# Kernel optimization log

Measured on AMD Instinct MI355X. Metric: run time of the kernel, lower is better.

## Reference

```python
import jax, jax.numpy as jnp
import numpy as np

B, T, D = 4, 1024, 768
HW = 32            # H = W = sqrt(T)
DS = D // 16       # d_state = 48
CHUNK = 8          # items_each_chunk (must divide W)


def _ln(x, w, b, eps=1e-5):
    mu = x.mean(-1, keepdims=True)
    var = ((x - mu) ** 2).mean(-1, keepdims=True)
    return (x - mu) / jnp.sqrt(var + eps) * w + b


def _conv1x1(x, w):  # x: (B,C,H,W), w: (O,C)
    return jnp.einsum('bchw,oc->bohw', x, w)


def _dwconv(x, w, b, pad):  # depthwise conv, w: (C,1,k,k)
    y = jax.lax.conv_general_dilated(
        x, w, (1, 1), [(pad, pad), (pad, pad)],
        dimension_numbers=('NCHW', 'OIHW', 'NCHW'),
        feature_group_count=x.shape[1])
    if b is not None:
        y = y + b[None, :, None, None]
    return y


def _norm_gates(Gl, Gm, Gr):
    gl, gm, gr = jax.nn.sigmoid(Gl), jax.nn.sigmoid(Gm), jax.nn.sigmoid(Gr)
    s = gl + gm + gr
    s = s.at[:, :, 0, :].set(gm[:, :, 0, :] + gr[:, :, 0, :])    # top row: no h-1 neighbor
    s = s.at[:, :, -1, :].set(gl[:, :, -1, :] + gm[:, :, -1, :])  # bottom row: no h+1 neighbor
    s = jnp.maximum(s, 1e-7)
    return gl / s, gm / s, gr / s


def _gspn_scan(X, L, Gl, Gm, Gr, chunk):
    # GateRecurrent2dnoind: scan along W in independent chunks of `chunk` columns.
    # H[:, :, h, t] = L*X + Gl*Hprev[h-1] + Gm*Hprev[h] + Gr*Hprev[h+1], Hprev=0 at chunk start.
    b, c, h, w = X.shape
    nc = w // chunk

    def to_scan(a):  # (B,C,H,W) -> (chunk, B, C, H, nc)
        return a.reshape(b, c, h, nc, chunk).transpose(4, 0, 1, 2, 3)

    xs, ls, gls, gms, grs = map(to_scan, (X, L, Gl, Gm, Gr))

    def step(hprev, inp):
        x, l, gl, gm, gr = inp
        h_up = jnp.pad(hprev[:, :, :-1], ((0, 0), (0, 0), (1, 0), (0, 0)))
        h_dn = jnp.pad(hprev[:, :, 1:], ((0, 0), (0, 0), (0, 1), (0, 0)))
        hn = l * x + gl * h_up + gm * hprev + gr * h_dn
        return hn, hn

    _, ys = jax.lax.scan(step, jnp.zeros((b, c, h, nc), X.dtype), (xs, ls, gls, gms, grs))
    return ys.transpose(1, 2, 3, 4, 0).reshape(b, c, h, w)


def setup_inputs() -> dict:
    key = jax.random.key(0)
    ks = jax.random.split(key, 16)
    s = 0.02
    return {
        'hidden_states': jax.random.normal(ks[0], (B, T, D), jnp.float32),
        'norm_w': jnp.ones((D,), jnp.float32),
        'norm_b': jnp.zeros((D,), jnp.float32),
        'in_proj_w': jax.random.normal(ks[1], (D, D), jnp.float32) * s,
        'conv7_w': jax.random.normal(ks[2], (D, 1, 7, 7), jnp.float32) * s,
        'conv7_b': jnp.zeros((D,), jnp.float32),
        'xdown_w': jax.random.normal(ks[3], (DS, D), jnp.float32) * s,
        'wup_w': jax.random.normal(ks[4], (12 * D, DS), jnp.float32) * s,
        'lup_w': jax.random.normal(ks[5], (4 * D, DS), jnp.float32) * s,
        'uup_w': jax.random.normal(ks[6], (4 * D, DS), jnp.float32) * s,
        'dcoef_w': jax.random.normal(ks[7], (4 * D, DS), jnp.float32) * s,
        'm_w': jax.random.normal(ks[8], (4,), jnp.float32) * 0.25,
        'outconv_w': jax.random.normal(ks[9], (D, D), jnp.float32) * s,
        'outdconv_w': jax.random.normal(ks[10], (D, 1, 3, 3), jnp.float32) * s,
        'outproj_w': jax.random.normal(ks[11], (D, D), jnp.float32) * s,
    }


def reference(hidden_states, norm_w, norm_b, in_proj_w, conv7_w, conv7_b,
              xdown_w, wup_w, lup_w, uup_w, dcoef_w, m_w,
              outconv_w, outdconv_w, outproj_w):
    b, t, d = hidden_states.shape
    hh = ww = HW
    shortcut = hidden_states
    x = _ln(shortcut, norm_w, norm_b)                      # (B,T,D)
    x = x.transpose(0, 2, 1).reshape(b, d, hh, ww)         # (B,D,H,W)
    x = _conv1x1(x, in_proj_w)
    x = _dwconv(x, conv7_w, conv7_b, 3)
    xp = _conv1x1(x, xdown_w)                              # (B,ds,H,W)
    ws = _conv1x1(xp, wup_w)                               # (B,12D,H,W)
    Ls = _conv1x1(xp, lup_w)                               # (B,4D,H,W)
    Us = _conv1x1(xp, uup_w)
    Ds = _conv1x1(xp, dcoef_w)
    # 4 scan directions: [x, x^T, flip_w(x), flip_w(x^T)]
    x_hwwh = jnp.stack([x, x.transpose(0, 1, 3, 2)], axis=1)       # (B,2,D,H,W)
    xs = jnp.concatenate([x_hwwh, x_hwwh[..., ::-1]], axis=1)      # (B,4,D,H,W)
    xs = xs.reshape(b, 4 * d, hh, ww)
    Gl, Gm, Gr = ws[:, :4 * d], ws[:, 4 * d:8 * d], ws[:, 8 * d:]
    gl, gm, gr = _norm_gates(Gl, Gm, Gr)
    out = _gspn_scan(xs, Ls, gl, gm, gr, CHUNK)
    out = out * Us + xs * Ds
    out = out.reshape(b, 4, d, hh, ww)
    out = jnp.einsum('bkdhw,k->bdhw', out, m_w)            # m_conv (1x1 over 4 dirs)
    out = _conv1x1(out, outconv_w)
    out = _dwconv(out, outdconv_w, None, 1)
    out = out * jax.nn.relu(out)
    out = out.reshape(b, d, t).transpose(0, 2, 1)
    out = out @ outproj_w.T
    return out, shortcut
```

## Files before the change

kernel.cpp:

```cpp
#include <hip/hip_runtime.h>

typedef unsigned short u16;
typedef unsigned int u32;
typedef __attribute__((ext_vector_type(8))) short short8v;
typedef __attribute__((ext_vector_type(4))) float f32x4;
typedef __attribute__((ext_vector_type(2))) unsigned u32x2v;

#define DD 768
#define PP 1024
#define NTOK 4096

__device__ __forceinline__ u16 f2bf(float f) {
  u32 u = __builtin_bit_cast(u32, f);
  u += 0x7fffu + ((u >> 16) & 1u);
  return (u16)(u >> 16);
}
__device__ __forceinline__ float b2f(u16 v) {
  return __builtin_bit_cast(float, (u32)v << 16);
}
__device__ __forceinline__ u32 pk_trunc(float fa, float fb) {
  return __builtin_amdgcn_perm(__builtin_bit_cast(u32, fa), __builtin_bit_cast(u32, fb), 0x07060302u);
}
__device__ __forceinline__ float ex8(const short8v& v, int j) {
  const u32 dw = ((const u32*)&v)[j >> 1];
  return __builtin_bit_cast(float, (j & 1) ? (dw & 0xffff0000u) : (dw << 16));
}
__device__ __forceinline__ float dpp_shr1(float x) {
  return __builtin_bit_cast(float,
      __builtin_amdgcn_update_dpp(0, __builtin_bit_cast(int, x), 0x138, 0xf, 0xf, true));
}
__device__ __forceinline__ float dpp_shl1(float x) {
  return __builtin_bit_cast(float,
      __builtin_amdgcn_update_dpp(0, __builtin_bit_cast(int, x), 0x130, 0xf, 0xf, true));
}
__device__ __forceinline__ float xhalf_sum(float p) {
#if __has_builtin(__builtin_amdgcn_permlane32_swap)
  u32x2v sw = __builtin_amdgcn_permlane32_swap(__builtin_bit_cast(u32, p),
                                               __builtin_bit_cast(u32, p), false, false);
  return __builtin_bit_cast(float, sw[0]) + __builtin_bit_cast(float, sw[1]);
#else
  return p + __shfl_xor(p, 32, 64);
#endif
}

__global__ __launch_bounds__(256) void prep_ln_k(const float* __restrict__ hs,
                                                 const float* __restrict__ gw, const float* __restrict__ gb,
                                                 u16* __restrict__ lnout, float* __restrict__ shortcut,
                                                 const float* __restrict__ win, u16* __restrict__ wInB,
                                                 const float* __restrict__ wout, u16* __restrict__ wOutB,
                                                 const float* __restrict__ wprj, u16* __restrict__ wPrjB,
                                                 const float* __restrict__ xdw, u16* __restrict__ wXdB,
                                                 const float* __restrict__ wup, const float* __restrict__ lup,
                                                 const float* __restrict__ uup, const float* __restrict__ dco,
                                                 u16* __restrict__ wB) {
  const int id = blockIdx.x;
  const int t = threadIdx.x;
  if (id < 4096) {
    const int tok = id;
    const float* xr = hs + (size_t)tok * DD;
    float v0 = xr[t], v1 = xr[t + 256], v2 = xr[t + 512];
    float s = v0 + v1 + v2;
    float q = v0 * v0 + v1 * v1 + v2 * v2;
#pragma unroll
    for (int off = 32; off > 0; off >>= 1) {
      s += __shfl_down(s, off, 64);
      q += __shfl_down(q, off, 64);
    }
    __shared__ float ss[4], qs[4];
    const int wid = t >> 6, lane = t & 63;
    if (lane == 0) { ss[wid] = s; qs[wid] = q; }
    __syncthreads();
    const float st = ss[0] + ss[1] + ss[2] + ss[3];
    const float qt = qs[0] + qs[1] + qs[2] + qs[3];
    const float mu = st * (1.f / 768.f);
    const float var = qt * (1.f / 768.f) - mu * mu;
    const float rstd = rsqrtf(var + 1e-5f);
    float* sc = shortcut + (size_t)tok * DD;
    u16* lo = lnout + (size_t)tok * DD;
    sc[t] = v0; sc[t + 256] = v1; sc[t + 512] = v2;
    lo[t]       = f2bf((v0 - mu) * rstd * gw[t] + gb[t]);
    lo[t + 256] = f2bf((v1 - mu) * rstd * gw[t + 256] + gb[t + 256]);
    lo[t + 512] = f2bf((v2 - mu) * rstd * gw[t + 512] + gb[t + 512]);
    return;
  }
  const int id2 = id - 4096;
  if (id2 < 1728) {
    const int m = id2 / 576;
    const int i = (id2 - m * 576) * 1024 + t * 4;
    const float* s = (m == 0) ? win : (m == 1) ? wout : wprj;
    u16* d = (m == 0) ? wInB : (m == 1) ? wOutB : wPrjB;
    const float4 v = *reinterpret_cast<const float4*>(s + i);
    u16 o[4] = {f2bf(v.x), f2bf(v.y), f2bf(v.z), f2bf(v.w)};
    *reinterpret_cast<uint2*>(d + i) = *reinterpret_cast<const uint2*>(o);
  } else if (id2 < 1776) {
    const int i = (id2 - 1728) * 1024 + t * 4;
    const int r = i / DD;
    if (r < 48) {
      const float4 v = *reinterpret_cast<const float4*>(xdw + i);
      u16 o[4] = {f2bf(v.x), f2bf(v.y), f2bf(v.z), f2bf(v.w)};
      *reinterpret_cast<uint2*>(wXdB + i) = *reinterpret_cast<const uint2*>(o);
    } else {
      *reinterpret_cast<uint2*>(wXdB + i) = make_uint2(0u, 0u);
    }
  } else {
    const int c = id2 - 1776;
    u16* dst = wB + (size_t)c * 2048;
    for (int i = t; i < 2048; i += 256) {
      const int row = i >> 6, s = i & 63;
      u16 v = 0;
      if (row < 24 && s < 48) {
        const int k = row & 3, type = row >> 2;
        const int ch = k * DD + c;
        const float* src;
        if (type < 3) src = wup + ((size_t)(type * 3072 + ch)) * 48;
        else if (type == 3) src = lup + (size_t)ch * 48;
        else if (type == 4) src = uup + (size_t)ch * 48;
        else src = dco + (size_t)ch * 48;
        v = f2bf(src[s]);
      }
      dst[i] = v;
    }
  }
}

template <int BSRC>
__global__ __launch_bounds__(256) void gemm_bf16(const u16* __restrict__ A,
                                                 const u16* __restrict__ Bt,
                                                 void* __restrict__ outv, const int mode) {
  __shared__ u16 Al[64][72];
  __shared__ u16 BlF[71 * 72];
  const int t = threadIdx.x;
  const int ntile = blockIdx.x * 64;
  const int mtile = blockIdx.y * 64;
  const int bb = ntile >> 10, pq0 = ntile & 1023;
  const int wid = t >> 6, lane = t & 63;
  const int m0 = (wid & 1) * 32, n0 = (wid >> 1) * 32;
  const int l15 = lane & 15, quad = lane >> 4;
  f32x4 acc[2][2];
#pragma unroll
  for (int mi = 0; mi < 2; ++mi)
#pragma unroll
    for (int ni = 0; ni < 2; ++ni) acc[mi][ni] = (f32x4){0.f, 0.f, 0.f, 0.f};
  const int ra = t >> 2, sa = t & 3;
  const u16* ag = A + (size_t)(mtile + ra) * DD + sa * 16;
  const int rb = t >> 2, hb = t & 3;
  const u16* bg = Bt + (size_t)(ntile + rb) * DD + hb * 16;
  const int chp = t >> 3, tok0 = (t & 7) * 8;
  const u16* bgc0 = Bt + ((size_t)(bb * DD + chp * 2)) * PP + pq0 + tok0;
  const u16* bgc1 = bgc0 + PP;
  uint4 pa0, pa1, pb0, pb1;
#define LOADK(k0)                                                              \
  {                                                                            \
    pa0 = *reinterpret_cast<const uint4*>(ag + (k0));                          \
    pa1 = *reinterpret_cast<const uint4*>(ag + (k0) + 8);                      \
    if (BSRC == 0) {                                                           \
      pb0 = *reinterpret_cast<const uint4*>(bg + (k0));                        \
      pb1 = *reinterpret_cast<const uint4*>(bg + (k0) + 8);                    \
    } else {                                                                   \
      pb0 = *reinterpret_cast<const uint4*>(bgc0 + (size_t)(k0) * PP);         \
      pb1 = *reinterpret_cast<const uint4*>(bgc1 + (size_t)(k0) * PP);         \
    }                                                                          \
  }
  LOADK(0);
  for (int k0 = 0; k0 < DD; k0 += 64) {
    __syncthreads();
    *reinterpret_cast<uint4*>(&Al[ra][sa * 16]) = pa0;
    *reinterpret_cast<uint4*>(&Al[ra][sa * 16 + 8]) = pa1;
    if (BSRC == 0) {
      const int pr = rb + (rb >> 3);
      *reinterpret_cast<uint4*>(&BlF[pr * 72 + hb * 16]) = pb0;
      *reinterpret_cast<uint4*>(&BlF[pr * 72 + hb * 16 + 8]) = pb1;
    } else {
      union { uint4 v; u16 u[8]; } ua, ub;
      ua.v = pb0; ub.v = pb1;
#pragma unroll
      for (int i2 = 0; i2 < 8; ++i2) {
        const int tk = tok0 + i2;
        const int prow = (tk + (tk >> 3)) * 72;
        *reinterpret_cast<u32*>(&BlF[prow + chp * 2]) =
            (u32)ua.u[i2] | ((u32)ub.u[i2] << 16);
      }
    }
    __syncthreads();
    if (k0 + 64 < DD) LOADK(k0 + 64);
    short8v af[2][2], bfr[2][2];
#pragma unroll
    for (int mi = 0; mi < 2; ++mi)
#pragma unroll
      for (int ks = 0; ks < 2; ++ks)
        af[mi][ks] = *reinterpret_cast<const short8v*>(&Al[m0 + mi * 16 + l15][ks * 32 + quad * 8]);
#pragma unroll
    for (int ni = 0; ni < 2; ++ni) {
      const int tl = n0 + ni * 16 + l15;
      const int prow = (tl + (tl >> 3)) * 72;
#pragma unroll
      for (int ks = 0; ks < 2; ++ks)
        bfr[ni][ks] = *reinterpret_cast<const short8v*>(&BlF[prow + ks * 32 + quad * 8]);
    }
#pragma unroll
    for (int mi = 0; mi < 2; ++mi)
#pragma unroll
      for (int ni = 0; ni < 2; ++ni) {
        acc[mi][ni] = __builtin_amdgcn_mfma_f32_16x16x32_bf16(af[mi][0], bfr[ni][0], acc[mi][ni], 0, 0, 0);
        acc[mi][ni] = __builtin_amdgcn_mfma_f32_16x16x32_bf16(af[mi][1], bfr[ni][1], acc[mi][ni], 0, 0, 0);
      }
  }
#undef LOADK
  if (mode == 1) {
#pragma unroll
    for (int mi = 0; mi < 2; ++mi)
#pragma unroll
      for (int ni = 0; ni < 2; ++ni) {
        const int ob = mtile + m0 + mi * 16 + quad * 4;
        const int pg = ntile + n0 + ni * 16 + l15;
        *reinterpret_cast<f32x4*>((float*)outv + (size_t)pg * DD + ob) = acc[mi][ni];
      }
  } else {
    __syncthreads();
#pragma unroll
    for (int mi = 0; mi < 2; ++mi)
#pragma unroll
      for (int ni = 0; ni < 2; ++ni)
#pragma unroll
        for (int r = 0; r < 4; ++r)
          BlF[(m0 + mi * 16 + quad * 4 + r) * 72 + n0 + ni * 16 + l15] = f2bf(acc[mi][ni][r]);
    __syncthreads();
    const int orow = t >> 2, oc0 = (t & 3) * 16;
    const uint4 o0 = *reinterpret_cast<const uint4*>(&BlF[orow * 72 + oc0]);
    const uint4 o1 = *reinterpret_cast<const uint4*>(&BlF[orow * 72 + oc0 + 8]);
    u16* dstb = (u16*)outv + ((size_t)(bb * DD + mtile + orow)) * PP + pq0 + oc0;
    *reinterpret_cast<uint4*>(dstb) = o0;
    *reinterpret_cast<uint4*>(dstb + 8) = o1;
  }
}

__global__ __launch_bounds__(256) void xdgemm_k(const u16* __restrict__ A,
                                                const u16* __restrict__ Ycm,
                                                u16* __restrict__ xpA) {
  __shared__ u16 Al[64][72];
  __shared__ u16 Bl[16][72];
  const int t = threadIdx.x;
  const int ntile = blockIdx.x * 16;
  const int bb = ntile >> 10, pq0 = ntile & 1023;
  const int wid = t >> 6, lane = t & 63, l15 = lane & 15, quad = lane >> 4;
  f32x4 acc = (f32x4){0.f, 0.f, 0.f, 0.f};
  const int arow = t >> 2, aks = (t & 3) * 16;
  const u16* ag = A + (size_t)arow * DD + aks;
  const int chp = t >> 3;
  const int tk0 = (t & 7) * 2;
  const u16* bg0 = Ycm + ((size_t)(bb * DD + chp * 2)) * PP + pq0 + tk0;
  uint4 pa0, pa1;
  u32 pb0, pb1;
#define LOADX(k0)                                                     \
  {                                                                   \
    pa0 = *reinterpret_cast<const uint4*>(ag + (k0));                 \
    pa1 = *reinterpret_cast<const uint4*>(ag + (k0) + 8);             \
    pb0 = *reinterpret_cast<const u32*>(bg0 + (size_t)(k0) * PP);     \
    pb1 = *reinterpret_cast<const u32*>(bg0 + (size_t)((k0) + 1) * PP); \
  }
  LOADX(0);
  for (int k0 = 0; k0 < DD; k0 += 64) {
    __syncthreads();
    *reinterpret_cast<uint4*>(&Al[arow][aks]) = pa0;
    *reinterpret_cast<uint4*>(&Al[arow][aks + 8]) = pa1;
    *reinterpret_cast<u32*>(&Bl[tk0][chp * 2]) = (pb0 & 0xffffu) | (pb1 << 16);
    *reinterpret_cast<u32*>(&Bl[tk0 + 1][chp * 2]) = (pb0 >> 16) | (pb1 & 0xffff0000u);
    __syncthreads();
    if (k0 + 64 < DD) LOADX(k0 + 64);
#pragma unroll
    for (int ks = 0; ks < 2; ++ks) {
      const short8v af = *reinterpret_cast<const short8v*>(&Al[wid * 16 + l15][ks * 32 + quad * 8]);
      const short8v bf = *reinterpret_cast<const short8v*>(&Bl[l15][ks * 32 + quad * 8]);
      acc = __builtin_amdgcn_mfma_f32_16x16x32_bf16(af, bf, acc, 0, 0, 0);
    }
  }
#undef LOADX
  const int pq = pq0 + l15;
  const int i = ((pq & 31) >> 4) * 512 + (pq >> 5) * 16 + (pq & 15);
  u16* dst = xpA + ((size_t)(bb * 1024 + i)) * 64 + wid * 16 + quad * 4;
  *reinterpret_cast<uint2*>(dst) = make_uint2(pk_trunc(acc[1], acc[0]), pk_trunc(acc[3], acc[2]));
}

__global__ __launch_bounds__(256) void dwconv7_k(const u16* __restrict__ x,
                                                 const float* __restrict__ wgt,
                                                 const float* __restrict__ bias,
                                                 u16* __restrict__ y) {
  const int bc = blockIdx.x;
  const int c = bc % DD;
  __shared__ float tile[38 * 38];
  __shared__ float wl[49];
  __shared__ float bsh[1];
  const int t = threadIdx.x;
  for (int i = t; i < 38 * 38; i += 256) tile[i] = 0.f;
  __syncthreads();
  const u16* xr = x + (size_t)bc * PP;
  for (int i = t; i < 512; i += 256) {
    const u32 v = reinterpret_cast<const u32*>(xr)[i];
    const int p0 = i * 2;
    const int h = p0 >> 5, w = p0 & 31;
    tile[(h + 3) * 38 + w + 3] = b2f((u16)v);
    tile[(h + 3) * 38 + w + 4] = b2f((u16)(v >> 16));
  }
  if (t < 49) wl[t] = wgt[c * 49 + t];
  if (t == 0) bsh[0] = bias[c];
  __syncthreads();
  u16* yo = y + (size_t)bc * PP;
  const int w = t & 31, hb = t >> 5;
  const float bv = bsh[0];
  float a0 = bv, a1 = bv, a2 = bv, a3 = bv;
#pragma unroll
  for (int rr = 0; rr < 10; ++rr) {
    float row[7];
#pragma unroll
    for (int kw = 0; kw < 7; ++kw) row[kw] = tile[(hb * 4 + rr) * 38 + w + kw];
    if (rr < 7) {
#pragma unroll
      for (int kw = 0; kw < 7; ++kw) a0 = fmaf(wl[rr * 7 + kw], row[kw], a0);
    }
    if (rr >= 1 && rr < 8) {
#pragma unroll
      for (int kw = 0; kw < 7; ++kw) a1 = fmaf(wl[(rr - 1) * 7 + kw], row[kw], a1);
    }
    if (rr >= 2 && rr < 9) {
#pragma unroll
      for (int kw = 0; kw < 7; ++kw) a2 = fmaf(wl[(rr - 2) * 7 + kw], row[kw], a2);
    }
    if (rr >= 3) {
#pragma unroll
      for (int kw = 0; kw < 7; ++kw) a3 = fmaf(wl[(rr - 3) * 7 + kw], row[kw], a3);
    }
  }
  yo[(hb * 4 + 0) * 32 + w] = f2bf(a0);
  yo[(hb * 4 + 1) * 32 + w] = f2bf(a1);
  yo[(hb * 4 + 2) * 32 + w] = f2bf(a2);
  yo[(hb * 4 + 3) * 32 + w] = f2bf(a3);
}

__global__ __launch_bounds__(256) void dwconv3_k(const u16* __restrict__ x,
                                                 const float* __restrict__ wgt,
                                                 u16* __restrict__ y) {
  const int bc = blockIdx.x;
  const int c = bc % DD;
  __shared__ float tile[34 * 34];
  __shared__ float wl[9];
  const int t = threadIdx.x;
  for (int i = t; i < 34 * 34; i += 256) tile[i] = 0.f;
  __syncthreads();
  const u16* xr = x + (size_t)bc * PP;
  for (int i = t; i < 512; i += 256) {
    const u32 v = reinterpret_cast<const u32*>(xr)[i];
    const int p0 = i * 2;
    const int h = p0 >> 5, w = p0 & 31;
    tile[(h + 1) * 34 + w + 1] = b2f((u16)v);
    tile[(h + 1) * 34 + w + 2] = b2f((u16)(v >> 16));
  }
  if (t < 9) wl[t] = wgt[c * 9 + t];
  __syncthreads();
  u16* yo = y + (size_t)bc * PP;
  const int w = t & 31, hb = t >> 5;
  float a0 = 0.f, a1 = 0.f, a2 = 0.f, a3 = 0.f;
#pragma unroll
  for (int rr = 0; rr < 6; ++rr) {
    float row[3];
#pragma unroll
    for (int kw = 0; kw < 3; ++kw) row[kw] = tile[(hb * 4 + rr) * 34 + w + kw];
    if (rr < 3) {
#pragma unroll
      for (int kw = 0; kw < 3; ++kw) a0 = fmaf(wl[rr * 3 + kw], row[kw], a0);
    }
    if (rr >= 1 && rr < 4) {
#pragma unroll
      for (int kw = 0; kw < 3; ++kw) a1 = fmaf(wl[(rr - 1) * 3 + kw], row[kw], a1);
    }
    if (rr >= 2 && rr < 5) {
#pragma unroll
      for (int kw = 0; kw < 3; ++kw) a2 = fmaf(wl[(rr - 2) * 3 + kw], row[kw], a2);
    }
    if (rr >= 3) {
#pragma unroll
      for (int kw = 0; kw < 3; ++kw) a3 = fmaf(wl[(rr - 3) * 3 + kw], row[kw], a3);
    }
  }
  const float r0 = a0 > 0.f ? a0 * a0 : 0.f;
  const float r1 = a1 > 0.f ? a1 * a1 : 0.f;
  const float r2 = a2 > 0.f ? a2 * a2 : 0.f;
  const float r3 = a3 > 0.f ? a3 * a3 : 0.f;
  yo[(hb * 4 + 0) * 32 + w] = f2bf(r0);
  yo[(hb * 4 + 1) * 32 + w] = f2bf(r1);
  yo[(hb * 4 + 2) * 32 + w] = f2bf(r2);
  yo[(hb * 4 + 3) * 32 + w] = f2bf(r3);
}

#define ACT_SWZ(row, col) ((col) ^ (((((col) >> 6) ^ (row)) & 7) << 3))
#define PSWZ(r) ((((r) ^ ((r) >> 3)) & 3) << 3)

__device__ __forceinline__ void produce_half(u16* __restrict__ actbuf,
                                             const u16* __restrict__ ab,
                                             const short8v bw[2][2],
                                             int l15, int quad, int g) {
#pragma unroll
  for (int mt = 0; mt < 8; ++mt) {
    const u16* ar = ab + (mt * 16 + l15) * 64 + quad * 8;
    const short8v a0 = *reinterpret_cast<const short8v*>(ar);
    const short8v a1 = *reinterpret_cast<const short8v*>(ar + 32);
    f32x4 acc0 = {0.f, 0.f, 0.f, 0.f}, acc1 = {0.f, 0.f, 0.f, 0.f};
    acc0 = __builtin_amdgcn_mfma_f32_16x16x32_bf16(a0, bw[0][0], acc0, 0, 0, 0);
    acc0 = __builtin_amdgcn_mfma_f32_16x16x32_bf16(a1, bw[0][1], acc0, 0, 0, 0);
    acc1 = __builtin_amdgcn_mfma_f32_16x16x32_bf16(a0, bw[1][0], acc1, 0, 0, 0);
    acc1 = __builtin_amdgcn_mfma_f32_16x16x32_bf16(a1, bw[1][1], acc1, 0, 0, 0);
    const int qb = g * 128 + mt * 16 + quad * 4;
    const int cs = ACT_SWZ(l15, qb);
    *reinterpret_cast<uint2*>(&actbuf[l15 * 512 + cs]) =
        make_uint2(pk_trunc(acc0[1], acc0[0]), pk_trunc(acc0[3], acc0[2]));
    if (l15 < 8)
      *reinterpret_cast<uint2*>(&actbuf[(16 + l15) * 512 + cs]) =
          make_uint2(pk_trunc(acc1[1], acc1[0]), pk_trunc(acc1[3], acc1[2]));
  }
}

__device__ __forceinline__ void consume_half(const u16* __restrict__ actbuf,
                                             const u16* __restrict__ planeTc,
                                             const u16* __restrict__ y2row,
                                             u16* __restrict__ outpc,
                                             float mw, int dpair, int cs2, int d, int h, int half) {
  __builtin_amdgcn_s_setprio(1);
  const int k = dpair * 2 + d;
  const int hc = half * 2 + cs2;
  const int colb = h * 16 + cs2 * 8;
  const int wst = dpair ? (24 - hc * 8) : (hc * 8);
  short8v vPr;
  if (d == 0) vPr = *reinterpret_cast<const short8v*>(y2row + h * 32 + wst);
  else        vPr = *reinterpret_cast<const short8v*>(planeTc + h * 40 + (wst ^ PSWZ(h)));
  short8v vPe;
  {
    const u32* s = (const u32*)&vPr;
    u32* dq = (u32*)&vPe;
    if (dpair) {
      dq[0] = (s[3] >> 16) | (s[3] << 16);
      dq[1] = (s[2] >> 16) | (s[2] << 16);
      dq[2] = (s[1] >> 16) | (s[1] << 16);
      dq[3] = (s[0] >> 16) | (s[0] << 16);
    } else {
      dq[0] = s[0]; dq[1] = s[1]; dq[2] = s[2]; dq[3] = s[3];
    }
  }
#define ACTP(row) (*reinterpret_cast<const short8v*>(&actbuf[(row) * 512 + ACT_SWZ((row), colb)]))
  const short8v vGl = ACTP(0 + k);
  const short8v vGm = ACTP(4 + k);
  const short8v vGr = ACTP(8 + k);
  const short8v vL  = ACTP(12 + k);
  const short8v vU  = ACTP(16 + k);
  const short8v vD  = ACTP(20 + k);
#undef ACTP
  const bool top = (h == 0), bot = (h == 31);
  float H = 0.f, prev = 0.f;
  u32 ox[4];
#pragma unroll
  for (int j = 0; j < 8; ++j) {
    float el = __expf(-ex8(vGl, j));
    const float em = __expf(-ex8(vGm, j));
    float er = __expf(-ex8(vGr, j));
    if (top) el = 1e30f;
    if (bot) er = 1e30f;
    const float pl2 = 1.f + el, pm = 1.f + em, pr = 1.f + er;
    const float ul = pm * pr, um = pl2 * pr, ur = pl2 * pm;
    const float rcpS = __builtin_amdgcn_rcpf(ul + um + ur);
    const float xv = ex8(vPe, j);
    const float Lx = ex8(vL, j) * xv;
    const float up = dpp_shr1(H);
    const float dn = dpp_shl1(H);
    H = fmaf(ul * rcpS, up, fmaf(um * rcpS, H, fmaf(ur * rcpS, dn, Lx)));
    float part = fmaf(H, ex8(vU, j), xv * ex8(vD, j)) * mw;
    part = xhalf_sum(part);
    if (j & 1) ox[j >> 1] = pk_trunc(part, prev);
    else prev = part;
  }
  if (d == 0) {
    uint4 o;
    o.x = ox[0]; o.y = ox[1]; o.z = ox[2]; o.w = ox[3];
    *reinterpret_cast<uint4*>(&outpc[h * 64 + dpair * 32 + ((hc * 8) ^ ((h & 3) << 3))]) = o;
  }
  __builtin_amdgcn_s_setprio(0);
}

__global__ __launch_bounds__(512, 4) void scan_k(const u16* __restrict__ y2b,
                                                 const u16* __restrict__ xpA,
                                                 const u16* __restrict__ wB,
                                                 const float* __restrict__ mwp,
                                                 u16* __restrict__ out1) {
  const int bc2 = blockIdx.x;
  const int b = bc2 / 384;
  const int cpair = bc2 - b * 384;
  const int c0 = cpair * 2;
  __shared__ __align__(16) u16 actA[24 * 512];
  __shared__ __align__(16) u16 actB[24 * 512];
  __shared__ __align__(16) u16 planeT[2][1280];
  __shared__ __align__(16) u16 outp[2][32 * 64];
  const int t = threadIdx.x;
  const int wid = t >> 6, lane = t & 63, l15 = lane & 15, quad = lane >> 4;
  const int ch = wid >> 2;
  const int g = wid & 3;
  const int dpair = g & 1, cs2 = g >> 1;
  const int d = lane >> 5, h = lane & 31;
  const int c = c0 + ch;
  const int bc = b * DD + c;
  {
    const int pch = t >> 8, idx = t & 255;
    const u16* yp = y2b + (size_t)(b * DD + c0 + pch) * PP;
#pragma unroll
    for (int i2 = 0; i2 < 2; ++i2) {
      const int i = idx + i2 * 256;
      const u32 v = reinterpret_cast<const u32*>(yp)[i];
      const int p0 = i * 2;
      const int hh = p0 >> 5, ww = p0 & 31;
      planeT[pch][ww * 40 + (hh ^ PSWZ(ww))] = (u16)v;
      planeT[pch][(ww + 1) * 40 + (hh ^ PSWZ(ww + 1))] = (u16)(v >> 16);
    }
  }
  const u16* wc = wB + (size_t)c * 2048;
  short8v bw[2][2];
#pragma unroll
  for (int nt = 0; nt < 2; ++nt)
#pragma unroll
    for (int ks = 0; ks < 2; ++ks)
      bw[nt][ks] = *reinterpret_cast<const short8v*>(wc + (nt * 16 + l15) * 64 + ks * 32 + quad * 8);
  const u16* xb = xpA + ((size_t)(b * 1024)) * 64;
  const u16* y2row = y2b + (size_t)bc * PP;
  const float mw = mwp[dpair * 2 + d];
  if (ch == 0) produce_half(actA, xb + (size_t)(g * 128) * 64, bw, l15, quad, g);
  __syncthreads();
  if (ch == 0) consume_half(actA, planeT[0], y2row, outp[0], mw, dpair, cs2, d, h, 0);
  else         produce_half(actB, xb + (size_t)(g * 128) * 64, bw, l15, quad, g);
  __syncthreads();
  if (ch == 1) consume_half(actB, planeT[1], y2row, outp[1], mw, dpair, cs2, d, h, 0);
  else         produce_half(actA, xb + (size_t)(512 + g * 128) * 64, bw, l15, quad, g);
  __syncthreads();
  if (ch == 0) consume_half(actA, planeT[0], y2row, outp[0], mw, dpair, cs2, d, h, 1);
  else         produce_half(actB, xb + (size_t)(512 + g * 128) * 64, bw, l15, quad, g);
  __syncthreads();
  if (ch == 1) consume_half(actB, planeT[1], y2row, outp[1], mw, dpair, cs2, d, h, 1);
  __syncthreads();
  const int hh2 = t >> 4, wp = t & 15;
  const int wsw = (wp * 2) ^ ((hh2 & 3) << 3);
#pragma unroll
  for (int cc = 0; cc < 2; ++cc) {
    const u32 u0 = *reinterpret_cast<const u32*>(&outp[cc][hh2 * 64 + wsw]);
    const u32 u1 = *reinterpret_cast<const u32*>(&outp[cc][hh2 * 64 + 32 + wsw]);
    const float v0 = b2f((u16)u0) + b2f((u16)u1);
    const float v1 = b2f((u16)(u0 >> 16)) + b2f((u16)(u1 >> 16));
    *reinterpret_cast<u32*>(out1 + (size_t)(b * DD + c0 + cc) * PP + hh2 * 32 + wp * 2) =
        pk_trunc(v1, v0);
  }
}

extern "C" void kernel_launch(void* const* d_in, const int* in_sizes, int n_in,
                              void* d_out, int out_size, void* d_ws, size_t ws_size,
                              hipStream_t stream) {
  const float* hs   = (const float*)d_in[0];
  const float* nw   = (const float*)d_in[1];
  const float* nb   = (const float*)d_in[2];
  const float* win  = (const float*)d_in[3];
  const float* c7w  = (const float*)d_in[4];
  const float* c7b  = (const float*)d_in[5];
  const float* xdw  = (const float*)d_in[6];
  const float* wupw = (const float*)d_in[7];
  const float* lupw = (const float*)d_in[8];
  const float* uupw = (const float*)d_in[9];
  const float* dcow = (const float*)d_in[10];
  const float* mww  = (const float*)d_in[11];
  const float* wout = (const float*)d_in[12];
  const float* odw  = (const float*)d_in[13];
  const float* wprj = (const float*)d_in[14];
  float* out0 = (float*)d_out;
  float* shortcut = out0 + (size_t)NTOK * DD;

  char* ws = (char*)d_ws;
  u16* lnA    = (u16*)(ws + 0);
  u16* wInB   = (u16*)(ws + 6291456);
  u16* wOutB  = (u16*)(ws + 7471104);
  u16* wPrjB  = (u16*)(ws + 8650752);
  u16* wB     = (u16*)(ws + 9830400);
  u16* wXdB   = (u16*)(ws + 12976128);
  u16* xpA    = (u16*)(ws + 13074432);
  u16* y1b    = (u16*)(ws + 13598720);
  u16* y2b    = (u16*)(ws + 19890176);
  u16* out1   = (u16*)(ws + 26181632);
  u16* y3b    = y1b;
  u16* y4b    = out1;

  prep_ln_k<<<6640, 256, 0, stream>>>(hs, nw, nb, lnA, shortcut,
                                      win, wInB, wout, wOutB, wprj, wPrjB,
                                      xdw, wXdB, wupw, lupw, uupw, dcow, wB);
  gemm_bf16<0><<<dim3(64, 12), 256, 0, stream>>>(wInB, lnA, y1b, 3);
  dwconv7_k<<<3072, 256, 0, stream>>>(y1b, c7w, c7b, y2b);
  xdgemm_k<<<256, 256, 0, stream>>>(wXdB, y2b, xpA);
  scan_k<<<1536, 512, 0, stream>>>(y2b, xpA, wB, mww, out1);
  gemm_bf16<1><<<dim3(64, 12), 256, 0, stream>>>(wOutB, out1, y3b, 3);
  dwconv3_k<<<3072, 256, 0, stream>>>(y3b, odw, y4b);
  gemm_bf16<1><<<dim3(64, 12), 256, 0, stream>>>(wPrjB, y4b, out0, 1);
}
```

Before: 221.5 us.

## Double-buffer LDS in gemm_bf16 and split-K the xdown GEMM across two groups

The three large GEMMs now use two LDS buffers, so the next K-tile is staged while the current one is computed, cutting the barriers per step from two to one. The xdown projection kernel runs 512 threads, split into two 256-thread halves that each reduce half of K, and their partial sums are combined through shared memory. The split aims to double parallelism for the small 256-block launch. The cost is extra LDS per block, which may reduce occupancy, plus one extra reduction pass.

```diff
diff --git a/kernel.cpp b/kernel.cpp
--- a/kernel.cpp
+++ b/kernel.cpp
@@ -127,8 +127,8 @@
 __global__ __launch_bounds__(256) void gemm_bf16(const u16* __restrict__ A,
                                                  const u16* __restrict__ Bt,
                                                  void* __restrict__ outv, const int mode) {
-  __shared__ u16 Al[64][72];
-  __shared__ u16 BlF[71 * 72];
+  __shared__ u16 Al[2][64 * 72];
+  __shared__ u16 BlF[2][71 * 72];
   const int t = threadIdx.x;
   const int ntile = blockIdx.x * 64;
   const int mtile = blockIdx.y * 64;
@@ -161,51 +161,70 @@
       pb1 = *reinterpret_cast<const uint4*>(bgc1 + (size_t)(k0) * PP);         \
     }                                                                          \
   }
+#define STAGE(buf)                                                             \
+  {                                                                            \
+    *reinterpret_cast<uint4*>(&Al[buf][ra * 72 + sa * 16]) = pa0;              \
+    *reinterpret_cast<uint4*>(&Al[buf][ra * 72 + sa * 16 + 8]) = pa1;          \
+    if (BSRC == 0) {                                                           \
+      const int pr_ = rb + (rb >> 3);                                          \
+      *reinterpret_cast<uint4*>(&BlF[buf][pr_ * 72 + hb * 16]) = pb0;          \
+      *reinterpret_cast<uint4*>(&BlF[buf][pr_ * 72 + hb * 16 + 8]) = pb1;      \
+    } else {                                                                   \
+      union { uint4 v; u16 u[8]; } ua_, ub_;                                   \
+      ua_.v = pb0; ub_.v = pb1;                                                \
+      _Pragma("unroll")                                                        \
+      for (int i2 = 0; i2 < 8; ++i2) {                                         \
+        const int tk_ = tok0 + i2;                                             \
+        const int prow_ = (tk_ + (tk_ >> 3)) * 72;                             \
+        *reinterpret_cast<u32*>(&BlF[buf][prow_ + chp * 2]) =                  \
+            (u32)ua_.u[i2] | ((u32)ub_.u[i2] << 16);                           \
+      }                                                                        \
+    }                                                                          \
+  }
+#define COMPUTE(buf)                                                           \
+  {                                                                            \
+    short8v af_[2][2], bfr_[2][2];                                             \
+    _Pragma("unroll")                                                          \
+    for (int mi = 0; mi < 2; ++mi)                                             \
+      _Pragma("unroll")                                                        \
+      for (int ks = 0; ks < 2; ++ks)                                           \
+        af_[mi][ks] = *reinterpret_cast<const short8v*>(                       \
+            &Al[buf][(m0 + mi * 16 + l15) * 72 + ks * 32 + quad * 8]);         \
+    _Pragma("unroll")                                                          \
+    for (int ni = 0; ni < 2; ++ni) {                                           \
+      const int tl_ = n0 + ni * 16 + l15;                                      \
+      const int prow_ = (tl_ + (tl_ >> 3)) * 72;                               \
+      _Pragma("unroll")                                                        \
+      for (int ks = 0; ks < 2; ++ks)                                           \
+        bfr_[ni][ks] = *reinterpret_cast<const short8v*>(                      \
+            &BlF[buf][prow_ + ks * 32 + quad * 8]);                            \
+    }                                                                          \
+    _Pragma("unroll")                                                          \
+    for (int mi = 0; mi < 2; ++mi)                                             \
+      _Pragma("unroll")                                                        \
+      for (int ni = 0; ni < 2; ++ni) {                                         \
+        acc[mi][ni] = __builtin_amdgcn_mfma_f32_16x16x32_bf16(                 \
+            af_[mi][0], bfr_[ni][0], acc[mi][ni], 0, 0, 0);                    \
+        acc[mi][ni] = __builtin_amdgcn_mfma_f32_16x16x32_bf16(                 \
+            af_[mi][1], bfr_[ni][1], acc[mi][ni], 0, 0, 0);                    \
+      }                                                                        \
+  }
   LOADK(0);
-  for (int k0 = 0; k0 < DD; k0 += 64) {
+  STAGE(0);
+  __syncthreads();
+  for (int k0 = 0; k0 < DD; k0 += 128) {
+    LOADK(k0 + 64);
+    COMPUTE(0);
+    STAGE(1);
     __syncthreads();
-    *reinterpret_cast<uint4*>(&Al[ra][sa * 16]) = pa0;
-    *reinterpret_cast<uint4*>(&Al[ra][sa * 16 + 8]) = pa1;
-    if (BSRC == 0) {
-      const int pr = rb + (rb >> 3);
-      *reinterpret_cast<uint4*>(&BlF[pr * 72 + hb * 16]) = pb0;
-      *reinterpret_cast<uint4*>(&BlF[pr * 72 + hb * 16 + 8]) = pb1;
-    } else {
-      union { uint4 v; u16 u[8]; } ua, ub;
-      ua.v = pb0; ub.v = pb1;
-#pragma unroll
-      for (int i2 = 0; i2 < 8; ++i2) {
-        const int tk = tok0 + i2;
-        const int prow = (tk + (tk >> 3)) * 72;
-        *reinterpret_cast<u32*>(&BlF[prow + chp * 2]) =
-            (u32)ua.u[i2] | ((u32)ub.u[i2] << 16);
-      }
-    }
+    if (k0 + 128 < DD) LOADK(k0 + 128);
+    COMPUTE(1);
+    if (k0 + 128 < DD) STAGE(0);
     __syncthreads();
-    if (k0 + 64 < DD) LOADK(k0 + 64);
-    short8v af[2][2], bfr[2][2];
-#pragma unroll
-    for (int mi = 0; mi < 2; ++mi)
-#pragma unroll
-      for (int ks = 0; ks < 2; ++ks)
-        af[mi][ks] = *reinterpret_cast<const short8v*>(&Al[m0 + mi * 16 + l15][ks * 32 + quad * 8]);
-#pragma unroll
-    for (int ni = 0; ni < 2; ++ni) {
-      const int tl = n0 + ni * 16 + l15;
-      const int prow = (tl + (tl >> 3)) * 72;
-#pragma unroll
-      for (int ks = 0; ks < 2; ++ks)
-        bfr[ni][ks] = *reinterpret_cast<const short8v*>(&BlF[prow + ks * 32 + quad * 8]);
-    }
-#pragma unroll
-    for (int mi = 0; mi < 2; ++mi)
-#pragma unroll
-      for (int ni = 0; ni < 2; ++ni) {
-        acc[mi][ni] = __builtin_amdgcn_mfma_f32_16x16x32_bf16(af[mi][0], bfr[ni][0], acc[mi][ni], 0, 0, 0);
-        acc[mi][ni] = __builtin_amdgcn_mfma_f32_16x16x32_bf16(af[mi][1], bfr[ni][1], acc[mi][ni], 0, 0, 0);
-      }
   }
 #undef LOADK
+#undef STAGE
+#undef COMPUTE
   if (mode == 1) {
 #pragma unroll
     for (int mi = 0; mi < 2; ++mi)
@@ -216,69 +235,83 @@
         *reinterpret_cast<f32x4*>((float*)outv + (size_t)pg * DD + ob) = acc[mi][ni];
       }
   } else {
-    __syncthreads();
 #pragma unroll
     for (int mi = 0; mi < 2; ++mi)
 #pragma unroll
       for (int ni = 0; ni < 2; ++ni)
 #pragma unroll
         for (int r = 0; r < 4; ++r)
-          BlF[(m0 + mi * 16 + quad * 4 + r) * 72 + n0 + ni * 16 + l15] = f2bf(acc[mi][ni][r]);
+          BlF[0][(m0 + mi * 16 + quad * 4 + r) * 72 + n0 + ni * 16 + l15] = f2bf(acc[mi][ni][r]);
     __syncthreads();
     const int orow = t >> 2, oc0 = (t & 3) * 16;
-    const uint4 o0 = *reinterpret_cast<const uint4*>(&BlF[orow * 72 + oc0]);
-    const uint4 o1 = *reinterpret_cast<const uint4*>(&BlF[orow * 72 + oc0 + 8]);
+    const uint4 o0 = *reinterpret_cast<const uint4*>(&BlF[0][orow * 72 + oc0]);
+    const uint4 o1 = *reinterpret_cast<const uint4*>(&BlF[0][orow * 72 + oc0 + 8]);
     u16* dstb = (u16*)outv + ((size_t)(bb * DD + mtile + orow)) * PP + pq0 + oc0;
     *reinterpret_cast<uint4*>(dstb) = o0;
     *reinterpret_cast<uint4*>(dstb + 8) = o1;
   }
 }
 
-__global__ __launch_bounds__(256) void xdgemm_k(const u16* __restrict__ A,
+__global__ __launch_bounds__(512) void xdgemm_k(const u16* __restrict__ A,
                                                 const u16* __restrict__ Ycm,
                                                 u16* __restrict__ xpA) {
-  __shared__ u16 Al[64][72];
-  __shared__ u16 Bl[16][72];
+  __shared__ u16 Al[2][64 * 72];
+  __shared__ u16 Bl[2][16 * 72];
+  __shared__ float Cmb[64][17];
   const int t = threadIdx.x;
+  const int gg = t >> 8;
+  const int t2 = t & 255;
   const int ntile = blockIdx.x * 16;
   const int bb = ntile >> 10, pq0 = ntile & 1023;
-  const int wid = t >> 6, lane = t & 63, l15 = lane & 15, quad = lane >> 4;
+  const int wid4 = t2 >> 6, lane = t & 63, l15 = lane & 15, quad = lane >> 4;
   f32x4 acc = (f32x4){0.f, 0.f, 0.f, 0.f};
-  const int arow = t >> 2, aks = (t & 3) * 16;
-  const u16* ag = A + (size_t)arow * DD + aks;
-  const int chp = t >> 3;
-  const int tk0 = (t & 7) * 2;
-  const u16* bg0 = Ycm + ((size_t)(bb * DD + chp * 2)) * PP + pq0 + tk0;
+  const int arow = t2 >> 2, aks = (t2 & 3) * 16;
+  const u16* ag = A + (size_t)arow * DD + gg * 384 + aks;
+  const int chp = t2 >> 3;
+  const int tk0 = (t2 & 7) * 2;
+  const u16* bg0 = Ycm + ((size_t)(bb * DD + chp * 2)) * PP + (size_t)(gg * 384) * PP + pq0 + tk0;
   uint4 pa0, pa1;
   u32 pb0, pb1;
-#define LOADX(k0)                                                     \
-  {                                                                   \
-    pa0 = *reinterpret_cast<const uint4*>(ag + (k0));                 \
-    pa1 = *reinterpret_cast<const uint4*>(ag + (k0) + 8);             \
-    pb0 = *reinterpret_cast<const u32*>(bg0 + (size_t)(k0) * PP);     \
+#define LOADX(k0)                                                       \
+  {                                                                     \
+    pa0 = *reinterpret_cast<const uint4*>(ag + (k0));                   \
+    pa1 = *reinterpret_cast<const uint4*>(ag + (k0) + 8);               \
+    pb0 = *reinterpret_cast<const u32*>(bg0 + (size_t)(k0) * PP);       \
     pb1 = *reinterpret_cast<const u32*>(bg0 + (size_t)((k0) + 1) * PP); \
   }
   LOADX(0);
-  for (int k0 = 0; k0 < DD; k0 += 64) {
+  for (int k0 = 0; k0 < 384; k0 += 64) {
     __syncthreads();
-    *reinterpret_cast<uint4*>(&Al[arow][aks]) = pa0;
-    *reinterpret_cast<uint4*>(&Al[arow][aks + 8]) = pa1;
-    *reinterpret_cast<u32*>(&Bl[tk0][chp * 2]) = (pb0 & 0xffffu) | (pb1 << 16);
-    *reinterpret_cast<u32*>(&Bl[tk0 + 1][chp * 2]) = (pb0 >> 16) | (pb1 & 0xffff0000u);
+    *reinterpret_cast<uint4*>(&Al[gg][arow * 72 + aks]) = pa0;
+    *reinterpret_cast<uint4*>(&Al[gg][arow * 72 + aks + 8]) = pa1;
+    *reinterpret_cast<u32*>(&Bl[gg][tk0 * 72 + chp * 2]) = (pb0 & 0xffffu) | (pb1 << 16);
+    *reinterpret_cast<u32*>(&Bl[gg][(tk0 + 1) * 72 + chp * 2]) = (pb0 >> 16) | (pb1 & 0xffff0000u);
     __syncthreads();
-    if (k0 + 64 < DD) LOADX(k0 + 64);
+    if (k0 + 64 < 384) LOADX(k0 + 64);
 #pragma unroll
     for (int ks = 0; ks < 2; ++ks) {
-      const short8v af = *reinterpret_cast<const short8v*>(&Al[wid * 16 + l15][ks * 32 + quad * 8]);
-      const short8v bf = *reinterpret_cast<const short8v*>(&Bl[l15][ks * 32 + quad * 8]);
+      const short8v af = *reinterpret_cast<const short8v*>(
+          &Al[gg][(wid4 * 16 + l15) * 72 + ks * 32 + quad * 8]);
+      const short8v bf = *reinterpret_cast<const short8v*>(
+          &Bl[gg][l15 * 72 + ks * 32 + quad * 8]);
       acc = __builtin_amdgcn_mfma_f32_16x16x32_bf16(af, bf, acc, 0, 0, 0);
     }
   }
 #undef LOADX
-  const int pq = pq0 + l15;
-  const int i = ((pq & 31) >> 4) * 512 + (pq >> 5) * 16 + (pq & 15);
-  u16* dst = xpA + ((size_t)(bb * 1024 + i)) * 64 + wid * 16 + quad * 4;
-  *reinterpret_cast<uint2*>(dst) = make_uint2(pk_trunc(acc[1], acc[0]), pk_trunc(acc[3], acc[2]));
+  __syncthreads();
+  if (gg == 1) {
+#pragma unroll
+    for (int r = 0; r < 4; ++r) Cmb[wid4 * 16 + quad * 4 + r][l15] = acc[r];
+  }
+  __syncthreads();
+  if (gg == 0) {
+#pragma unroll
+    for (int r = 0; r < 4; ++r) acc[r] += Cmb[wid4 * 16 + quad * 4 + r][l15];
+    const int pq = pq0 + l15;
+    const int i = ((pq & 31) >> 4) * 512 + (pq >> 5) * 16 + (pq & 15);
+    u16* dst = xpA + ((size_t)(bb * 1024 + i)) * 64 + wid4 * 16 + quad * 4;
+    *reinterpret_cast<uint2*>(dst) = make_uint2(pk_trunc(acc[1], acc[0]), pk_trunc(acc[3], acc[2]));
+  }
 }
 
 __global__ __launch_bounds__(256) void dwconv7_k(const u16* __restrict__ x,
@@ -593,7 +626,7 @@
                                       xdw, wXdB, wupw, lupw, uupw, dcow, wB);
   gemm_bf16<0><<<dim3(64, 12), 256, 0, stream>>>(wInB, lnA, y1b, 3);
   dwconv7_k<<<3072, 256, 0, stream>>>(y1b, c7w, c7b, y2b);
-  xdgemm_k<<<256, 256, 0, stream>>>(wXdB, y2b, xpA);
+  xdgemm_k<<<256, 512, 0, stream>>>(wXdB, y2b, xpA);
   scan_k<<<1536, 512, 0, stream>>>(y2b, xpA, wB, mww, out1);
   gemm_bf16<1><<<dim3(64, 12), 256, 0, stream>>>(wOutB, out1, y3b, 3);
   dwconv3_k<<<3072, 256, 0, stream>>>(y3b, odw, y4b);
```

Measured after the change: 222.1 us. Within noise of the previous version (+0.3%).
